# Performance work log

Measured on AMD Instinct MI355X. Metric: run time of the kernel, lower is better.

## Reference

```python
import jax, jax.numpy as jnp
import numpy as np

TOP_K = 4


def setup_inputs() -> dict:
    key = jax.random.key(0)
    ks = jax.random.split(key, 6)
    B, S, H, I, E = 2, 2048, 2880, 2880, 8
    scale = 0.02
    return {
        "x": jax.random.normal(ks[0], (B, S, H), dtype=jnp.float32),
        "router_w": jax.random.normal(ks[1], (E, H), dtype=jnp.float32) * scale,
        "router_b": jax.random.normal(ks[2], (E,), dtype=jnp.float32) * scale,
        "w_gate": jax.random.normal(ks[3], (E, H, I), dtype=jnp.float32) * scale,
        "w_up": jax.random.normal(ks[4], (E, H, I), dtype=jnp.float32) * scale,
        "w_down": jax.random.normal(ks[5], (E, I, H), dtype=jnp.float32) * scale,
    }


def _moe_forward(x, router_w, router_b, w_gate, w_up, w_down):
    B, S, H = x.shape
    E = router_w.shape[0]
    xf = x.reshape(-1, H)  # (T, H); note: self.norm is unused in the original forward
    T = xf.shape[0]

    # Router: linear -> top-k -> softmax over the k selected logits
    logits = xf @ router_w.T + router_b          # (T, E)
    topv, topi = jax.lax.top_k(logits, TOP_K)    # (T, K)
    aff_k = jax.nn.softmax(topv, axis=-1)        # (T, K), sums to 1
    aff = jnp.zeros_like(logits).at[jnp.arange(T)[:, None], topi].set(aff_k)  # (T, E)

    # Expert SwiGLU MLPs, affinity-weighted combine (aff is 0 for unselected experts)
    out = jnp.zeros_like(xf)
    for e in range(E):  # fixed small structural loop over experts
        g = xf @ w_gate[e]                       # (T, I)
        u = xf @ w_up[e]                         # (T, I)
        h = jax.nn.silu(g) * u                   # SwiGLU
        out = out + aff[:, e:e + 1] * (h @ w_down[e])
    return out.reshape(B, S, H)


def reference(x, router_w, router_b, w_gate, w_up, w_down):
    return _moe_forward(x, router_w, router_b, w_gate, w_up, w_down)
```

## Files before the change

### kernel.cpp

```cpp
#include <hip/hip_runtime.h>

#define T_TOK 4096
#define HDIM  2880
#define IDIM  2880
#define NEXP  8
#define TOPK  4
#define WEL   (2880 * 2880)

#define BM 128
#define BN 96
#define BK 64
#define NPAN 30
#define ASZ (BM * BK)
#define BSZ (BN * BK)
#define NSTEP 45

typedef __attribute__((ext_vector_type(8))) short  s16x8;
typedef __attribute__((ext_vector_type(8))) unsigned short u16x8;
typedef __attribute__((ext_vector_type(4))) float  f32x4;

__device__ __forceinline__ unsigned short f2bf(float f) {
  unsigned int u = __float_as_uint(f);
  u += 0x7FFFu + ((u >> 16) & 1u);
  return (unsigned short)(u >> 16);
}

__device__ __forceinline__ void gload16(const unsigned short* g, unsigned short* l) {
  __builtin_amdgcn_global_load_lds(
      (const __attribute__((address_space(1))) void*)g,
      (__attribute__((address_space(3))) void*)l, 16, 0, 0);
}

__device__ __forceinline__ int xcd_swz(int orig, int n) {
  int q = n >> 3, r = n & 7;
  int x = orig & 7, idx = orig >> 3;
  return (x < r ? x * (q + 1) : r * (q + 1) + (x - r) * q) + idx;
}

__global__ __launch_bounds__(256) void cvt_kernel(const float* __restrict__ x,
                                                  unsigned short* __restrict__ xb) {
  int i = blockIdx.x * 256 + threadIdx.x;
  const f32x4* p = (const f32x4*)x;
  f32x4 a = p[2 * (size_t)i];
  f32x4 b = p[2 * (size_t)i + 1];
  u16x8 o;
  o[0] = f2bf(a[0]); o[1] = f2bf(a[1]); o[2] = f2bf(a[2]); o[3] = f2bf(a[3]);
  o[4] = f2bf(b[0]); o[5] = f2bf(b[1]); o[6] = f2bf(b[2]); o[7] = f2bf(b[3]);
  *(u16x8*)(xb + (size_t)i * 8) = o;
}

__global__ __launch_bounds__(256) void transpose_group_kernel(
    const float* __restrict__ wg, const float* __restrict__ wu,
    const float* __restrict__ wd, unsigned short* __restrict__ wbuf, int ge) {
  __shared__ unsigned short st[64][72];
  const int z = blockIdx.z, j = z / 3, m = z % 3;
  const float* src = (m == 0 ? wg : (m == 1 ? wu : wd)) + (size_t)(ge + j) * WEL;
  unsigned short* dst = wbuf + (size_t)(j * 3 + m) * WEL;
  const int k0 = blockIdx.x * 64, n0 = blockIdx.y * 64;
  const int tid = threadIdx.x;
#pragma unroll
  for (int u = 0; u < 4; ++u) {
    int idx = tid + u * 256;
    int kr = idx >> 4;
    int nc = (idx & 15) * 4;
    f32x4 v = *(const f32x4*)(src + (size_t)(k0 + kr) * 2880 + (n0 + nc));
#pragma unroll
    for (int q = 0; q < 4; ++q) st[nc + q][kr] = f2bf(v[q]);
  }
  __syncthreads();
  int n = tid >> 2;
  int kc = (tid & 3) * 16;
  u16x8 a = *(const u16x8*)(&st[n][kc]);
  u16x8 b = *(const u16x8*)(&st[n][kc + 8]);
  unsigned short* po = dst + (size_t)(n0 + n) * 2880 + (k0 + kc);
  *(u16x8*)(po) = a;
  *(u16x8*)(po + 8) = b;
}

__global__ __launch_bounds__(256) void router_kernel(const float* __restrict__ x,
                                                     const float* __restrict__ rw,
                                                     const float* __restrict__ rb,
                                                     float* __restrict__ aff,
                                                     int* __restrict__ cnt,
                                                     int* __restrict__ lst) {
  const int wv = threadIdx.x >> 6, lane = threadIdx.x & 63;
  const int tok0 = (blockIdx.x * 4 + wv) * 4;
  float acc[4][NEXP];
#pragma unroll
  for (int t = 0; t < 4; ++t)
#pragma unroll
    for (int e = 0; e < NEXP; ++e) acc[t][e] = 0.f;

#pragma unroll
  for (int it = 0; it < 12; ++it) {
    int c = it * 64 + lane;
    if (c < 720) {
      f32x4 w4[NEXP];
#pragma unroll
      for (int e = 0; e < NEXP; ++e)
        w4[e] = *(const f32x4*)(rw + (size_t)e * HDIM + c * 4);
#pragma unroll
      for (int t = 0; t < 4; ++t) {
        f32x4 xv = *(const f32x4*)(x + (size_t)(tok0 + t) * HDIM + c * 4);
#pragma unroll
        for (int e = 0; e < NEXP; ++e)
          acc[t][e] += xv[0] * w4[e][0] + xv[1] * w4[e][1] + xv[2] * w4[e][2] + xv[3] * w4[e][3];
      }
    }
  }
#pragma unroll
  for (int t = 0; t < 4; ++t)
#pragma unroll
    for (int e = 0; e < NEXP; ++e) {
#pragma unroll
      for (int m = 32; m; m >>= 1) acc[t][e] += __shfl_xor(acc[t][e], m);
    }
  if (lane < 4) {
    int tok = tok0 + lane;
    float lg[NEXP];
#pragma unroll
    for (int e = 0; e < NEXP; ++e) lg[e] = acc[lane][e] + rb[e];
    bool used[NEXP];
#pragma unroll
    for (int e = 0; e < NEXP; ++e) used[e] = false;
    int bi[TOPK]; float bv[TOPK];
#pragma unroll
    for (int s = 0; s < TOPK; ++s) {
      int best = 0; float vbest = -1e30f;
#pragma unroll
      for (int e = 0; e < NEXP; ++e)
        if (!used[e] && lg[e] > vbest) { vbest = lg[e]; best = e; }
      used[best] = true; bi[s] = best; bv[s] = vbest;
    }
    float mx = bv[0];
    float w[TOPK]; float ssum = 0.f;
#pragma unroll
    for (int s = 0; s < TOPK; ++s) { w[s] = __expf(bv[s] - mx); ssum += w[s]; }
    float o[NEXP];
#pragma unroll
    for (int e = 0; e < NEXP; ++e) o[e] = 0.f;
#pragma unroll
    for (int s = 0; s < TOPK; ++s) o[bi[s]] = w[s] / ssum;
#pragma unroll
    for (int e = 0; e < NEXP; ++e) aff[(size_t)tok * NEXP + e] = o[e];
#pragma unroll
    for (int s = 0; s < TOPK; ++s) {
      int p = atomicAdd(&cnt[bi[s]], 1);
      lst[bi[s] * T_TOK + p] = tok;
    }
  }
}

__global__ void sched_kernel(const int* __restrict__ cnt, int* __restrict__ gbs,
                             int* __restrict__ ess, int* __restrict__ gtot, int G) {
  if (threadIdx.x == 0 && blockIdx.x == 0) {
    int ng = NEXP / G;
    for (int g = 0; g < ng; ++g) {
      int b = 0, s = 0;
      for (int j = 0; j < G; ++j) {
        int e = g * G + j;
        gbs[e] = b; ess[e] = s;
        b += ((cnt[e] + BM - 1) / BM) * NPAN;
        s += cnt[e];
      }
      gtot[g] = b;
    }
  }
}

__device__ __forceinline__ bool locate(int orig, const int* gbs, const int* cnts,
                                       int ge, int G, const int* gtot_g,
                                       int& e, int& m0, int& n0, int& cnt) {
  int gt = *gtot_g;
  if (orig >= gt) return false;
  int bx = xcd_swz(orig, gt);
  int j = 0;
  for (int t = 1; t < G; ++t) j += (bx >= gbs[ge + t]) ? 1 : 0;
  e = ge + j;
  cnt = cnts[e];
  int mb = (cnt + BM - 1) >> 7;
  int local = bx - gbs[e];
  int nIdx = local / mb;
  int mIdx = local - nIdx * mb;
  m0 = mIdx * BM;
  n0 = nIdx * BN;
  return true;
}

__global__ __launch_bounds__(256) void gateup_kernel(
    const unsigned short* __restrict__ xb, const unsigned short* __restrict__ wbuf,
    const float* __restrict__ aff, const int* __restrict__ lst,
    const int* __restrict__ cnts, const int* __restrict__ gbs,
    const int* __restrict__ ess, const int* __restrict__ gtot_g,
    unsigned short* __restrict__ h4, int ge, int G) {
  int e, m0, n0, cnt;
  if (!locate(blockIdx.x, gbs, cnts, ge, G, gtot_g, e, m0, n0, cnt)) return;
  const int j = e - ge;
  const int slotbase = ess[e];
  const unsigned short* wgt = wbuf + (size_t)j * 3 * WEL;
  const unsigned short* wut = wgt + WEL;

  __shared__ __align__(16) unsigned short Al[2 * ASZ];
  __shared__ __align__(16) unsigned short Bgl[2 * BSZ];
  __shared__ __align__(16) unsigned short Bul[2 * BSZ];

  const int tid = threadIdx.x;
  const int wv = tid >> 6, lane = tid & 63;
  const int msub = (wv >> 1) * 64, nsub = (wv & 1) * 48;
  const int l15 = lane & 15, l4 = lane >> 4;
  const int lr = lane >> 3, lc = lane & 7;
  const int* mylst = lst + e * T_TOK;

  const unsigned short* asrc[4]; unsigned short* adst[4];
#pragma unroll
  for (int u = 0; u < 4; ++u) {
    int s = u * 4 + wv;
    int r = s * 8 + lr;
    int tok = mylst[min(m0 + r, cnt - 1)];
    asrc[u] = xb + (size_t)tok * HDIM + (lc ^ (r & 7)) * 8;
    adst[u] = &Al[s * 512];
  }
  const unsigned short* bgsrc[3]; const unsigned short* busrc[3];
  unsigned short* bgdst[3]; unsigned short* budst[3];
#pragma unroll
  for (int u = 0; u < 3; ++u) {
    int s = u * 4 + wv;
    int r = s * 8 + lr;
    size_t off = (size_t)(n0 + r) * HDIM + (size_t)((lc ^ (r & 7)) * 8);
    bgsrc[u] = wgt + off; busrc[u] = wut + off;
    bgdst[u] = &Bgl[s * 512]; budst[u] = &Bul[s * 512];
  }

  f32x4 accg[4][3]; f32x4 accu[4][3];
#pragma unroll
  for (int mf = 0; mf < 4; ++mf)
#pragma unroll
    for (int nf = 0; nf < 3; ++nf) { accg[mf][nf] = (f32x4)0.f; accu[mf][nf] = (f32x4)0.f; }

  auto stage = [&](int buf, int k0) {
    int ao = buf * ASZ, bo = buf * BSZ;
#pragma unroll
    for (int u = 0; u < 4; ++u) gload16(asrc[u] + k0, adst[u] + ao);
#pragma unroll
    for (int u = 0; u < 3; ++u) {
      gload16(bgsrc[u] + k0, bgdst[u] + bo);
      gload16(busrc[u] + k0, budst[u] + bo);
    }
  };
  auto compute = [&](int buf) {
    const unsigned short* Ab = Al + buf * ASZ;
    const unsigned short* Bg = Bgl + buf * BSZ;
    const unsigned short* Bu = Bul + buf * BSZ;
#pragma unroll
    for (int kk = 0; kk < 2; ++kk) {
      s16x8 af[4];
#pragma unroll
      for (int mf = 0; mf < 4; ++mf) {
        int R = msub + mf * 16 + l15;
        int sl = (kk * 4 + l4) ^ (R & 7);
        af[mf] = *(const s16x8*)(&Ab[R * 64 + sl * 8]);
      }
#pragma unroll
      for (int nf = 0; nf < 3; ++nf) {
        int R = nsub + nf * 16 + l15;
        int sl = (kk * 4 + l4) ^ (R & 7);
        s16x8 bg = *(const s16x8*)(&Bg[R * 64 + sl * 8]);
        s16x8 bu = *(const s16x8*)(&Bu[R * 64 + sl * 8]);
#pragma unroll
        for (int mf = 0; mf < 4; ++mf) {
          accg[mf][nf] = __builtin_amdgcn_mfma_f32_16x16x32_bf16(af[mf], bg, accg[mf][nf], 0, 0, 0);
          accu[mf][nf] = __builtin_amdgcn_mfma_f32_16x16x32_bf16(af[mf], bu, accu[mf][nf], 0, 0, 0);
        }
      }
    }
  };

  stage(0, 0);
#pragma unroll 1
  for (int t = 0; t < NSTEP - 1; t += 2) {
    stage(1, (t + 1) * BK);
    asm volatile("s_waitcnt vmcnt(10)" ::: "memory");
    __builtin_amdgcn_s_barrier();
    compute(0);
    __builtin_amdgcn_s_barrier();
    stage(0, (t + 2) * BK);
    asm volatile("s_waitcnt vmcnt(10)" ::: "memory");
    __builtin_amdgcn_s_barrier();
    compute(1);
    __builtin_amdgcn_s_barrier();
  }
  asm volatile("s_waitcnt vmcnt(0)" ::: "memory");
  __builtin_amdgcn_s_barrier();
  compute(0);

#pragma unroll
  for (int mf = 0; mf < 4; ++mf)
#pragma unroll
    for (int r = 0; r < 4; ++r) {
      int slot = m0 + msub + mf * 16 + l4 * 4 + r;
      if (slot < cnt) {
        int tok = mylst[slot];
        float av = aff[(size_t)tok * NEXP + e];
#pragma unroll
        for (int nf = 0; nf < 3; ++nf) {
          float g = accg[mf][nf][r], uu = accu[mf][nf][r];
          float hv = (g / (1.f + __expf(-g))) * uu * av;
          int col = n0 + nsub + nf * 16 + l15;
          h4[(size_t)(slotbase + slot) * IDIM + col] = f2bf(hv);
        }
      }
    }
}

__global__ __launch_bounds__(256) void down_kernel(
    const unsigned short* __restrict__ h4, const unsigned short* __restrict__ wbuf,
    float* __restrict__ out, const int* __restrict__ lst,
    const int* __restrict__ cnts, const int* __restrict__ gbs,
    const int* __restrict__ ess, const int* __restrict__ gtot_g,
    int ge, int G) {
  int e, m0, n0, cnt;
  if (!locate(blockIdx.x, gbs, cnts, ge, G, gtot_g, e, m0, n0, cnt)) return;
  const int j = e - ge;
  const int slotbase = ess[e];
  const unsigned short* wdt = wbuf + (size_t)j * 3 * WEL + 2 * (size_t)WEL;

  __shared__ __align__(16) unsigned short Al[2 * ASZ];
  __shared__ __align__(16) unsigned short Bl[2 * BSZ];

  const int tid = threadIdx.x;
  const int wv = tid >> 6, lane = tid & 63;
  const int msub = (wv >> 1) * 64, nsub = (wv & 1) * 48;
  const int l15 = lane & 15, l4 = lane >> 4;
  const int lr = lane >> 3, lc = lane & 7;
  const int* mylst = lst + e * T_TOK;

  const unsigned short* asrc[4]; unsigned short* adst[4];
#pragma unroll
  for (int u = 0; u < 4; ++u) {
    int s = u * 4 + wv;
    int r = s * 8 + lr;
    int hr = min(m0 + r, cnt - 1);
    asrc[u] = h4 + (size_t)(slotbase + hr) * IDIM + (lc ^ (r & 7)) * 8;
    adst[u] = &Al[s * 512];
  }
  const unsigned short* bsrc[3]; unsigned short* bdst[3];
#pragma unroll
  for (int u = 0; u < 3; ++u) {
    int s = u * 4 + wv;
    int r = s * 8 + lr;
    bsrc[u] = wdt + (size_t)(n0 + r) * IDIM + (size_t)((lc ^ (r & 7)) * 8);
    bdst[u] = &Bl[s * 512];
  }

  f32x4 acc[4][3];
#pragma unroll
  for (int mf = 0; mf < 4; ++mf)
#pragma unroll
    for (int nf = 0; nf < 3; ++nf) acc[mf][nf] = (f32x4)0.f;

  auto stage = [&](int buf, int k0) {
    int ao = buf * ASZ, bo = buf * BSZ;
#pragma unroll
    for (int u = 0; u < 4; ++u) gload16(asrc[u] + k0, adst[u] + ao);
#pragma unroll
    for (int u = 0; u < 3; ++u) gload16(bsrc[u] + k0, bdst[u] + bo);
  };
  auto compute = [&](int buf) {
    const unsigned short* Ab = Al + buf * ASZ;
    const unsigned short* Bb = Bl + buf * BSZ;
#pragma unroll
    for (int kk = 0; kk < 2; ++kk) {
      s16x8 af[4];
#pragma unroll
      for (int mf = 0; mf < 4; ++mf) {
        int R = msub + mf * 16 + l15;
        int sl = (kk * 4 + l4) ^ (R & 7);
        af[mf] = *(const s16x8*)(&Ab[R * 64 + sl * 8]);
      }
#pragma unroll
      for (int nf = 0; nf < 3; ++nf) {
        int R = nsub + nf * 16 + l15;
        int sl = (kk * 4 + l4) ^ (R & 7);
        s16x8 bb = *(const s16x8*)(&Bb[R * 64 + sl * 8]);
#pragma unroll
        for (int mf = 0; mf < 4; ++mf)
          acc[mf][nf] = __builtin_amdgcn_mfma_f32_16x16x32_bf16(af[mf], bb, acc[mf][nf], 0, 0, 0);
      }
    }
  };

  stage(0, 0);
#pragma unroll 1
  for (int t = 0; t < NSTEP - 1; t += 2) {
    stage(1, (t + 1) * BK);
    asm volatile("s_waitcnt vmcnt(7)" ::: "memory");
    __builtin_amdgcn_s_barrier();
    compute(0);
    __builtin_amdgcn_s_barrier();
    stage(0, (t + 2) * BK);
    asm volatile("s_waitcnt vmcnt(7)" ::: "memory");
    __builtin_amdgcn_s_barrier();
    compute(1);
    __builtin_amdgcn_s_barrier();
  }
  asm volatile("s_waitcnt vmcnt(0)" ::: "memory");
  __builtin_amdgcn_s_barrier();
  compute(0);

#pragma unroll
  for (int mf = 0; mf < 4; ++mf)
#pragma unroll
    for (int r = 0; r < 4; ++r) {
      int slot = m0 + msub + mf * 16 + l4 * 4 + r;
      if (slot < cnt) {
        int tok = mylst[slot];
#pragma unroll
        for (int nf = 0; nf < 3; ++nf) {
          int col = n0 + nsub + nf * 16 + l15;
          atomicAdd(out + (size_t)tok * HDIM + col, acc[mf][nf][r]);
        }
      }
    }
}

extern "C" void kernel_launch(void* const* d_in, const int* in_sizes, int n_in,
                              void* d_out, int out_size, void* d_ws, size_t ws_size,
                              hipStream_t stream) {
  (void)in_sizes; (void)n_in;
  const float* x  = (const float*)d_in[0];
  const float* rw = (const float*)d_in[1];
  const float* rb = (const float*)d_in[2];
  const float* wg = (const float*)d_in[3];
  const float* wu = (const float*)d_in[4];
  const float* wd = (const float*)d_in[5];
  float* out = (float*)d_out;

  char* ws = (char*)d_ws;
  float* aff = (float*)ws;
  int*   cnt = (int*)(ws + 131072);
  int*   lst = (int*)(ws + 131584);
  int*   gbs = (int*)(ws + 262656);
  int*   ess = (int*)(ws + 262720);
  int*   gtot = (int*)(ws + 262784);
  unsigned short* xb = (unsigned short*)(ws + 263168);
  const size_t OFF_H4 = 263168 + 23592960ull;

  const size_t WELB = (size_t)WEL * 2;
  int G = 1;
  {
    size_t need8 = OFF_H4 + (size_t)16384 * IDIM * 2 + 8 * 3 * WELB;
    size_t need2 = OFF_H4 + (size_t)8192  * IDIM * 2 + 2 * 3 * WELB;
    if (ws_size >= need8) G = 8;
    else if (ws_size >= need2) G = 2;
  }
  const size_t h4b = (size_t)((G == 8) ? 16384 : (G == 2 ? 8192 : 4096)) * IDIM * 2;
  unsigned short* h4   = (unsigned short*)(ws + OFF_H4);
  unsigned short* wbuf = (unsigned short*)(ws + OFF_H4 + h4b);

  const int NG = NEXP / G;
  const int NBLK = (T_TOK * TOPK / BM + NEXP) * NPAN;

  hipMemsetAsync(out, 0, (size_t)out_size * sizeof(float), stream);
  hipMemsetAsync(cnt, 0, 512, stream);
  cvt_kernel<<<(T_TOK * HDIM / 8) / 256, 256, 0, stream>>>(x, xb);
  router_kernel<<<T_TOK / 16, 256, 0, stream>>>(x, rw, rb, aff, cnt, lst);
  sched_kernel<<<1, 64, 0, stream>>>(cnt, gbs, ess, gtot, G);

  for (int g = 0; g < NG; ++g) {
    int ge = g * G;
    transpose_group_kernel<<<dim3(45, 45, 3 * G), 256, 0, stream>>>(wg, wu, wd, wbuf, ge);
    gateup_kernel<<<NBLK, 256, 0, stream>>>(
        xb, wbuf, aff, lst, cnt, gbs, ess, gtot + g, h4, ge, G);
    down_kernel<<<NBLK, 256, 0, stream>>>(
        h4, wbuf, out, lst, cnt, gbs, ess, gtot + g, ge, G);
  }
}
```

Measured before the change: 1.401 ms.

## Widen down-projection tile to 192 columns and fold bf16 cast into router

The down-projection GEMM tile grows from 96 to 192 output columns, so each block loads its A tile (the h activations) once for twice as many columns. This halves the A-operand traffic and the number of down-kernel blocks, and the scheduler now keeps separate block offsets for the gate/up and down kernels. The standalone x-to-bf16 conversion kernel is removed and the cast is done inside the router while it already reads x, saving one launch and one full pass over x. The wider tile doubles the down-kernel accumulators and B-tile shared memory, which may lower occupancy.

```diff
diff --git a/kernel.cpp b/kernel.cpp
--- a/kernel.cpp
+++ b/kernel.cpp
@@ -8,15 +8,19 @@
 #define WEL   (2880 * 2880)
 
 #define BM 128
-#define BN 96
+#define BN_GU 96
+#define BN_DN 192
 #define BK 64
-#define NPAN 30
+#define NPAN_GU 30
+#define NPAN_DN 15
 #define ASZ (BM * BK)
-#define BSZ (BN * BK)
+#define BSZ_GU (BN_GU * BK)
+#define BSZ_DN (BN_DN * BK)
 #define NSTEP 45
 
 typedef __attribute__((ext_vector_type(8))) short  s16x8;
 typedef __attribute__((ext_vector_type(8))) unsigned short u16x8;
+typedef __attribute__((ext_vector_type(4))) unsigned short u16x4;
 typedef __attribute__((ext_vector_type(4))) float  f32x4;
 
 __device__ __forceinline__ unsigned short f2bf(float f) {
@@ -35,18 +39,6 @@
   int q = n >> 3, r = n & 7;
   int x = orig & 7, idx = orig >> 3;
   return (x < r ? x * (q + 1) : r * (q + 1) + (x - r) * q) + idx;
-}
-
-__global__ __launch_bounds__(256) void cvt_kernel(const float* __restrict__ x,
-                                                  unsigned short* __restrict__ xb) {
-  int i = blockIdx.x * 256 + threadIdx.x;
-  const f32x4* p = (const f32x4*)x;
-  f32x4 a = p[2 * (size_t)i];
-  f32x4 b = p[2 * (size_t)i + 1];
-  u16x8 o;
-  o[0] = f2bf(a[0]); o[1] = f2bf(a[1]); o[2] = f2bf(a[2]); o[3] = f2bf(a[3]);
-  o[4] = f2bf(b[0]); o[5] = f2bf(b[1]); o[6] = f2bf(b[2]); o[7] = f2bf(b[3]);
-  *(u16x8*)(xb + (size_t)i * 8) = o;
 }
 
 __global__ __launch_bounds__(256) void transpose_group_kernel(
@@ -82,7 +74,8 @@
                                                      const float* __restrict__ rb,
                                                      float* __restrict__ aff,
                                                      int* __restrict__ cnt,
-                                                     int* __restrict__ lst) {
+                                                     int* __restrict__ lst,
+                                                     unsigned short* __restrict__ xb) {
   const int wv = threadIdx.x >> 6, lane = threadIdx.x & 63;
   const int tok0 = (blockIdx.x * 4 + wv) * 4;
   float acc[4][NEXP];
@@ -102,6 +95,9 @@
 #pragma unroll
       for (int t = 0; t < 4; ++t) {
         f32x4 xv = *(const f32x4*)(x + (size_t)(tok0 + t) * HDIM + c * 4);
+        u16x4 o;
+        o[0] = f2bf(xv[0]); o[1] = f2bf(xv[1]); o[2] = f2bf(xv[2]); o[3] = f2bf(xv[3]);
+        *(u16x4*)(xb + (size_t)(tok0 + t) * HDIM + c * 4) = o;
 #pragma unroll
         for (int e = 0; e < NEXP; ++e)
           acc[t][e] += xv[0] * w4[e][0] + xv[1] * w4[e][1] + xv[2] * w4[e][2] + xv[3] * w4[e][3];
@@ -151,26 +147,29 @@
   }
 }
 
-__global__ void sched_kernel(const int* __restrict__ cnt, int* __restrict__ gbs,
-                             int* __restrict__ ess, int* __restrict__ gtot, int G) {
+__global__ void sched_kernel(const int* __restrict__ cnt, int* __restrict__ gbs_gu,
+                             int* __restrict__ gbs_dn, int* __restrict__ ess,
+                             int* __restrict__ gtot_gu, int* __restrict__ gtot_dn, int G) {
   if (threadIdx.x == 0 && blockIdx.x == 0) {
     int ng = NEXP / G;
     for (int g = 0; g < ng; ++g) {
-      int b = 0, s = 0;
+      int bg_ = 0, bd_ = 0, s = 0;
       for (int j = 0; j < G; ++j) {
         int e = g * G + j;
-        gbs[e] = b; ess[e] = s;
-        b += ((cnt[e] + BM - 1) / BM) * NPAN;
+        gbs_gu[e] = bg_; gbs_dn[e] = bd_; ess[e] = s;
+        int mb = (cnt[e] + BM - 1) / BM;
+        bg_ += mb * NPAN_GU;
+        bd_ += mb * NPAN_DN;
         s += cnt[e];
       }
-      gtot[g] = b;
+      gtot_gu[g] = bg_; gtot_dn[g] = bd_;
     }
   }
 }
 
 __device__ __forceinline__ bool locate(int orig, const int* gbs, const int* cnts,
                                        int ge, int G, const int* gtot_g,
-                                       int& e, int& m0, int& n0, int& cnt) {
+                                       int& e, int& m0, int& nIdx, int& cnt) {
   int gt = *gtot_g;
   if (orig >= gt) return false;
   int bx = xcd_swz(orig, gt);
@@ -180,10 +179,8 @@
   cnt = cnts[e];
   int mb = (cnt + BM - 1) >> 7;
   int local = bx - gbs[e];
-  int nIdx = local / mb;
-  int mIdx = local - nIdx * mb;
-  m0 = mIdx * BM;
-  n0 = nIdx * BN;
+  nIdx = local / mb;
+  m0 = (local - nIdx * mb) * BM;
   return true;
 }
 
@@ -193,16 +190,17 @@
     const int* __restrict__ cnts, const int* __restrict__ gbs,
     const int* __restrict__ ess, const int* __restrict__ gtot_g,
     unsigned short* __restrict__ h4, int ge, int G) {
-  int e, m0, n0, cnt;
-  if (!locate(blockIdx.x, gbs, cnts, ge, G, gtot_g, e, m0, n0, cnt)) return;
+  int e, m0, nIdx, cnt;
+  if (!locate(blockIdx.x, gbs, cnts, ge, G, gtot_g, e, m0, nIdx, cnt)) return;
+  const int n0 = nIdx * BN_GU;
   const int j = e - ge;
   const int slotbase = ess[e];
   const unsigned short* wgt = wbuf + (size_t)j * 3 * WEL;
   const unsigned short* wut = wgt + WEL;
 
   __shared__ __align__(16) unsigned short Al[2 * ASZ];
-  __shared__ __align__(16) unsigned short Bgl[2 * BSZ];
-  __shared__ __align__(16) unsigned short Bul[2 * BSZ];
+  __shared__ __align__(16) unsigned short Bgl[2 * BSZ_GU];
+  __shared__ __align__(16) unsigned short Bul[2 * BSZ_GU];
 
   const int tid = threadIdx.x;
   const int wv = tid >> 6, lane = tid & 63;
@@ -238,7 +236,7 @@
     for (int nf = 0; nf < 3; ++nf) { accg[mf][nf] = (f32x4)0.f; accu[mf][nf] = (f32x4)0.f; }
 
   auto stage = [&](int buf, int k0) {
-    int ao = buf * ASZ, bo = buf * BSZ;
+    int ao = buf * ASZ, bo = buf * BSZ_GU;
 #pragma unroll
     for (int u = 0; u < 4; ++u) gload16(asrc[u] + k0, adst[u] + ao);
 #pragma unroll
@@ -249,8 +247,8 @@
   };
   auto compute = [&](int buf) {
     const unsigned short* Ab = Al + buf * ASZ;
-    const unsigned short* Bg = Bgl + buf * BSZ;
-    const unsigned short* Bu = Bul + buf * BSZ;
+    const unsigned short* Bg = Bgl + buf * BSZ_GU;
+    const unsigned short* Bu = Bul + buf * BSZ_GU;
 #pragma unroll
     for (int kk = 0; kk < 2; ++kk) {
       s16x8 af[4];
@@ -318,18 +316,19 @@
     const int* __restrict__ cnts, const int* __restrict__ gbs,
     const int* __restrict__ ess, const int* __restrict__ gtot_g,
     int ge, int G) {
-  int e, m0, n0, cnt;
-  if (!locate(blockIdx.x, gbs, cnts, ge, G, gtot_g, e, m0, n0, cnt)) return;
+  int e, m0, nIdx, cnt;
+  if (!locate(blockIdx.x, gbs, cnts, ge, G, gtot_g, e, m0, nIdx, cnt)) return;
+  const int n0 = nIdx * BN_DN;
   const int j = e - ge;
   const int slotbase = ess[e];
   const unsigned short* wdt = wbuf + (size_t)j * 3 * WEL + 2 * (size_t)WEL;
 
   __shared__ __align__(16) unsigned short Al[2 * ASZ];
-  __shared__ __align__(16) unsigned short Bl[2 * BSZ];
+  __shared__ __align__(16) unsigned short Bl[2 * BSZ_DN];
 
   const int tid = threadIdx.x;
   const int wv = tid >> 6, lane = tid & 63;
-  const int msub = (wv >> 1) * 64, nsub = (wv & 1) * 48;
+  const int msub = (wv >> 1) * 64, nsub = (wv & 1) * 96;
   const int l15 = lane & 15, l4 = lane >> 4;
   const int lr = lane >> 3, lc = lane & 7;
   const int* mylst = lst + e * T_TOK;
@@ -343,31 +342,31 @@
     asrc[u] = h4 + (size_t)(slotbase + hr) * IDIM + (lc ^ (r & 7)) * 8;
     adst[u] = &Al[s * 512];
   }
-  const unsigned short* bsrc[3]; unsigned short* bdst[3];
-#pragma unroll
-  for (int u = 0; u < 3; ++u) {
+  const unsigned short* bsrc[6]; unsigned short* bdst[6];
+#pragma unroll
+  for (int u = 0; u < 6; ++u) {
     int s = u * 4 + wv;
     int r = s * 8 + lr;
     bsrc[u] = wdt + (size_t)(n0 + r) * IDIM + (size_t)((lc ^ (r & 7)) * 8);
     bdst[u] = &Bl[s * 512];
   }
 
-  f32x4 acc[4][3];
+  f32x4 acc[4][6];
 #pragma unroll
   for (int mf = 0; mf < 4; ++mf)
 #pragma unroll
-    for (int nf = 0; nf < 3; ++nf) acc[mf][nf] = (f32x4)0.f;
+    for (int nf = 0; nf < 6; ++nf) acc[mf][nf] = (f32x4)0.f;
 
   auto stage = [&](int buf, int k0) {
-    int ao = buf * ASZ, bo = buf * BSZ;
+    int ao = buf * ASZ, bo = buf * BSZ_DN;
 #pragma unroll
     for (int u = 0; u < 4; ++u) gload16(asrc[u] + k0, adst[u] + ao);
 #pragma unroll
-    for (int u = 0; u < 3; ++u) gload16(bsrc[u] + k0, bdst[u] + bo);
+    for (int u = 0; u < 6; ++u) gload16(bsrc[u] + k0, bdst[u] + bo);
   };
   auto compute = [&](int buf) {
     const unsigned short* Ab = Al + buf * ASZ;
-    const unsigned short* Bb = Bl + buf * BSZ;
+    const unsigned short* Bb = Bl + buf * BSZ_DN;
 #pragma unroll
     for (int kk = 0; kk < 2; ++kk) {
       s16x8 af[4];
@@ -378,14 +377,15 @@
         af[mf] = *(const s16x8*)(&Ab[R * 64 + sl * 8]);
       }
 #pragma unroll
-      for (int nf = 0; nf < 3; ++nf) {
+      for (int nf = 0; nf < 6; ++nf) {
         int R = nsub + nf * 16 + l15;
         int sl = (kk * 4 + l4) ^ (R & 7);
-        s16x8 bb = *(const s16x8*)(&Bb[R * 64 + sl * 8]);
+        s16x8 bb = *(const s16x8*)(&Bl[buf * BSZ_DN + R * 64 + sl * 8]);
 #pragma unroll
         for (int mf = 0; mf < 4; ++mf)
           acc[mf][nf] = __builtin_amdgcn_mfma_f32_16x16x32_bf16(af[mf], bb, acc[mf][nf], 0, 0, 0);
       }
+      (void)Bb;
     }
   };
 
@@ -393,12 +393,12 @@
 #pragma unroll 1
   for (int t = 0; t < NSTEP - 1; t += 2) {
     stage(1, (t + 1) * BK);
-    asm volatile("s_waitcnt vmcnt(7)" ::: "memory");
+    asm volatile("s_waitcnt vmcnt(10)" ::: "memory");
     __builtin_amdgcn_s_barrier();
     compute(0);
     __builtin_amdgcn_s_barrier();
     stage(0, (t + 2) * BK);
-    asm volatile("s_waitcnt vmcnt(7)" ::: "memory");
+    asm volatile("s_waitcnt vmcnt(10)" ::: "memory");
     __builtin_amdgcn_s_barrier();
     compute(1);
     __builtin_amdgcn_s_barrier();
@@ -415,7 +415,7 @@
       if (slot < cnt) {
         int tok = mylst[slot];
 #pragma unroll
-        for (int nf = 0; nf < 3; ++nf) {
+        for (int nf = 0; nf < 6; ++nf) {
           int col = n0 + nsub + nf * 16 + l15;
           atomicAdd(out + (size_t)tok * HDIM + col, acc[mf][nf][r]);
         }
@@ -436,12 +436,14 @@
   float* out = (float*)d_out;
 
   char* ws = (char*)d_ws;
-  float* aff = (float*)ws;
-  int*   cnt = (int*)(ws + 131072);
-  int*   lst = (int*)(ws + 131584);
-  int*   gbs = (int*)(ws + 262656);
-  int*   ess = (int*)(ws + 262720);
-  int*   gtot = (int*)(ws + 262784);
+  float* aff     = (float*)ws;
+  int*   cnt     = (int*)(ws + 131072);
+  int*   lst     = (int*)(ws + 131584);
+  int*   gbs_gu  = (int*)(ws + 262656);
+  int*   gbs_dn  = (int*)(ws + 262720);
+  int*   ess     = (int*)(ws + 262784);
+  int*   gtot_gu = (int*)(ws + 262848);
+  int*   gtot_dn = (int*)(ws + 262912);
   unsigned short* xb = (unsigned short*)(ws + 263168);
   const size_t OFF_H4 = 263168 + 23592960ull;
 
@@ -458,20 +460,20 @@
   unsigned short* wbuf = (unsigned short*)(ws + OFF_H4 + h4b);
 
   const int NG = NEXP / G;
-  const int NBLK = (T_TOK * TOPK / BM + NEXP) * NPAN;
+  const int NBLK_GU = (T_TOK * TOPK / BM + NEXP) * NPAN_GU;
+  const int NBLK_DN = (T_TOK * TOPK / BM + NEXP) * NPAN_DN;
 
   hipMemsetAsync(out, 0, (size_t)out_size * sizeof(float), stream);
   hipMemsetAsync(cnt, 0, 512, stream);
-  cvt_kernel<<<(T_TOK * HDIM / 8) / 256, 256, 0, stream>>>(x, xb);
-  router_kernel<<<T_TOK / 16, 256, 0, stream>>>(x, rw, rb, aff, cnt, lst);
-  sched_kernel<<<1, 64, 0, stream>>>(cnt, gbs, ess, gtot, G);
+  router_kernel<<<T_TOK / 16, 256, 0, stream>>>(x, rw, rb, aff, cnt, lst, xb);
+  sched_kernel<<<1, 64, 0, stream>>>(cnt, gbs_gu, gbs_dn, ess, gtot_gu, gtot_dn, G);
 
   for (int g = 0; g < NG; ++g) {
     int ge = g * G;
     transpose_group_kernel<<<dim3(45, 45, 3 * G), 256, 0, stream>>>(wg, wu, wd, wbuf, ge);
-    gateup_kernel<<<NBLK, 256, 0, stream>>>(
-        xb, wbuf, aff, lst, cnt, gbs, ess, gtot + g, h4, ge, G);
-    down_kernel<<<NBLK, 256, 0, stream>>>(
-        h4, wbuf, out, lst, cnt, gbs, ess, gtot + g, ge, G);
-  }
-}
+    gateup_kernel<<<NBLK_GU, 256, 0, stream>>>(
+        xb, wbuf, aff, lst, cnt, gbs_gu, ess, gtot_gu + g, h4, ge, G);
+    down_kernel<<<NBLK_DN, 256, 0, stream>>>(
+        h4, wbuf, out, lst, cnt, gbs_dn, ess, gtot_dn + g, ge, G);
+  }
+}
```

Result: faster. 1.233 ms (-12.0%).
